# Performance work log

Measured on AMD Instinct MI355X. Metric: run time of the kernel, lower is better.

The kernel has to match this reference:

```python
import jax, jax.numpy as jnp
import numpy as np
from jax import lax
from jax.scipy.special import logsumexp

B, S, H, L = 64, 512, 1024, 9

def setup_inputs() -> dict:
    key = jax.random.key(0)
    ks = jax.random.split(key, 7)
    return {
        'sequence_output': jax.random.normal(ks[0], (B, S, H), dtype=jnp.float32),
        'tags': jax.random.randint(ks[1], (B, S), 0, L, dtype=jnp.int32),
        'mask': jnp.ones((B, S), dtype=bool),
        'W': jax.random.normal(ks[2], (L, H), dtype=jnp.float32) * 0.02,
        'b': jax.random.normal(ks[3], (L,), dtype=jnp.float32) * 0.02,
        'start_transitions': jax.random.normal(ks[4], (L,), dtype=jnp.float32) * 0.1,
        'end_transitions': jax.random.normal(ks[5], (L,), dtype=jnp.float32) * 0.1,
        'transitions': jax.random.normal(ks[6], (L,), dtype=jnp.float32).repeat(1) if False else jax.random.normal(ks[6], (L, L), dtype=jnp.float32) * 0.1,
    }

def _crf_nll(emissions, tags, mask, start_transitions, end_transitions, transitions):
    # emissions: [B,S,L], tags: [B,S] int, mask: [B,S] bool (mask[:,0] all True)
    Bn, Sn, Ln = emissions.shape
    maskf = mask.astype(emissions.dtype)
    bidx = jnp.arange(Bn)
    # ---- numerator: score of the gold tag sequence ----
    score = start_transitions[tags[:, 0]] + emissions[bidx, 0, tags[:, 0]]
    trans_sc = transitions[tags[:, :-1], tags[:, 1:]]                      # [B,S-1]
    emit_sc = jnp.take_along_axis(emissions, tags[..., None].astype(jnp.int32), axis=2)[..., 0]  # [B,S]
    score = score + jnp.sum((trans_sc + emit_sc[:, 1:]) * maskf[:, 1:], axis=1)
    seq_ends = jnp.sum(mask.astype(jnp.int32), axis=1) - 1                 # [B]
    last_tags = tags[bidx, seq_ends]
    score = score + end_transitions[last_tags]
    # ---- denominator: log partition via forward algorithm (scan over time) ----
    em_t = jnp.swapaxes(emissions, 0, 1)   # [S,B,L]
    mk_t = jnp.swapaxes(mask, 0, 1)        # [S,B]
    alpha0 = start_transitions + em_t[0]   # [B,L]
    def step(alpha, xs):
        em, m = xs
        nxt = logsumexp(alpha[:, :, None] + transitions[None] + em[:, None, :], axis=1)
        alpha = jnp.where(m[:, None], nxt, alpha)
        return alpha, None
    alpha, _ = lax.scan(step, alpha0, (em_t[1:], mk_t[1:]))
    logZ = logsumexp(alpha + end_transitions, axis=1)  # [B]
    llh = jnp.sum(score - logZ)  # reduction='sum'
    return -llh

def reference(sequence_output, tags, mask, W, b, start_transitions, end_transitions, transitions):
    # dropout is identity in eval/reference mode
    emissions = jnp.einsum('bsh,lh->bsl', sequence_output, W) + b
    return _crf_nll(emissions, tags, mask, start_transitions, end_transitions, transitions)
```

## Files before the change

kernel.cpp:

```cpp
#include <hip/hip_runtime.h>
#include <math.h>

#define Bn 64
#define Sn 512
#define Hn 1024
#define Ln 9
#define NC 32
#define KC 16

typedef __attribute__((ext_vector_type(8))) short bf16x8;
typedef __attribute__((ext_vector_type(4))) float f32x4;

__device__ __forceinline__ unsigned pack_bf16(float a, float b) {
  return (__float_as_uint(a) >> 16) | (__float_as_uint(b) & 0xFFFF0000u);
}

__global__ __launch_bounds__(256, 4) void crf_fused(
    const float* __restrict__ seq, const int* __restrict__ tags,
    const float* __restrict__ W, const float* __restrict__ bias,
    const float* __restrict__ startT, const float* __restrict__ endT,
    const float* __restrict__ trans, float* __restrict__ Mall,
    float* __restrict__ alphaBuf, float* __restrict__ out) {
  const int bc = blockIdx.x;
  const int b = bc >> 5, c = bc & (NC - 1);
  const int tid = threadIdx.x;
  const int lane = tid & 63;
  const int wv = tid >> 6;

  __shared__ float Clds[4][16][16];
  __shared__ float em_lds[KC][Ln];
  __shared__ float Mlds[2][Ln][12];

  const int t0 = c * KC;
  const int m = lane & 15;
  const int quad = lane >> 4;

  const float* arow = seq + ((size_t)b * Sn + t0 + m) * Hn;
  const bool bvalid = (m < Ln);
  const float* brow = W + (size_t)(bvalid ? m : 0) * Hn;

  f32x4 acc = {0.f, 0.f, 0.f, 0.f};
  const int ks = wv * 256;

#pragma unroll
  for (int it = 0; it < 8; ++it) {
    const int k0 = ks + it * 32 + quad * 8;
    float4 xa = *(const float4*)(arow + k0);
    float4 xb = *(const float4*)(arow + k0 + 4);
    float4 wa = *(const float4*)(brow + k0);
    float4 wb = *(const float4*)(brow + k0 + 4);

    union { bf16x8 v; unsigned u[4]; } af, bf;
    af.u[0] = pack_bf16(xa.x, xa.y);
    af.u[1] = pack_bf16(xa.z, xa.w);
    af.u[2] = pack_bf16(xb.x, xb.y);
    af.u[3] = pack_bf16(xb.z, xb.w);
    if (bvalid) {
      bf.u[0] = pack_bf16(wa.x, wa.y);
      bf.u[1] = pack_bf16(wa.z, wa.w);
      bf.u[2] = pack_bf16(wb.x, wb.y);
      bf.u[3] = pack_bf16(wb.z, wb.w);
    } else {
      bf.u[0] = bf.u[1] = bf.u[2] = bf.u[3] = 0u;
    }
    acc = __builtin_amdgcn_mfma_f32_16x16x32_bf16(af.v, bf.v, acc, 0, 0, 0);
  }

#pragma unroll
  for (int r = 0; r < 4; ++r) Clds[wv][quad * 4 + r][m] = acc[r];
  __syncthreads();

  if (tid < KC * Ln) {
    const int t = tid / Ln, l = tid - t * Ln;
    em_lds[t][l] = Clds[0][t][l] + Clds[1][t][l] + Clds[2][t][l] +
                   Clds[3][t][l] + bias[l];
  }
  __syncthreads();

  if (wv == 3) {
    float g = 0.f;
    if (lane < KC) {
      const int t = t0 + lane;
      const int cur = tags[b * Sn + t];
      const float e = em_lds[lane][cur];
      if (t == 0) {
        g = startT[cur] + e;
      } else {
        const int prev = tags[b * Sn + t - 1];
        g = trans[prev * Ln + cur] + e;
      }
      if (t == Sn - 1) g += endT[cur];
    }
#pragma unroll
    for (int off = 8; off > 0; off >>= 1) g += __shfl_xor(g, off);
    if (lane == 0) atomicAdd(out, -g);
  }

  if (c == 0) {
    if (wv == 0) {
      const int j = (lane < Ln) ? lane : 0;
      float Tcol[Ln];
#pragma unroll
      for (int i = 0; i < Ln; ++i) Tcol[i] = trans[i * Ln + j];
      float alpha[Ln];
#pragma unroll
      for (int i = 0; i < Ln; ++i) alpha[i] = startT[i] + em_lds[0][i];

      for (int t = 1; t < KC; ++t) {
        float mm = alpha[0];
#pragma unroll
        for (int i = 1; i < Ln; ++i) mm = fmaxf(mm, alpha[i]);
        float s = 0.f;
#pragma unroll
        for (int i = 0; i < Ln; ++i) s += __expf(alpha[i] - mm + Tcol[i]);
        float nxt = mm + __logf(s) + em_lds[t][j];
#pragma unroll
        for (int i = 0; i < Ln; ++i) alpha[i] = __shfl(nxt, i);
      }
      if (lane < Ln) alphaBuf[b * 16 + lane] = alpha[lane];
    }
  } else {
    const bool act = (tid < 81);
    const int i = tid / 9, j = tid - i * 9;
    float Treg[Ln];
    if (act) {
#pragma unroll
      for (int k = 0; k < Ln; ++k) Treg[k] = trans[k * Ln + j];
    }
    float val = 0.f;
    if (act) {
      val = trans[i * Ln + j] + em_lds[0][j];
      Mlds[0][i][j] = val;
    }
    __syncthreads();

    int cur = 0;
    for (int t = 1; t < KC; ++t) {
      if (act) {
        float Mr[Ln];
#pragma unroll
        for (int k = 0; k < Ln; ++k) Mr[k] = Mlds[cur][i][k];
        float e = em_lds[t][j];
        float mm = Mr[0];
#pragma unroll
        for (int k = 1; k < Ln; ++k) mm = fmaxf(mm, Mr[k]);
        float s = 0.f;
#pragma unroll
        for (int k = 0; k < Ln; ++k) s += __expf(Mr[k] - mm + Treg[k]);
        val = mm + __logf(s) + e;
        Mlds[cur ^ 1][i][j] = val;
      }
      __syncthreads();
      cur ^= 1;
    }
    if (act) Mall[(size_t)bc * 81 + tid] = val;
  }
}

__global__ __launch_bounds__(64) void crf_combine(
    const float* __restrict__ Mall, const float* __restrict__ alphaBuf,
    const float* __restrict__ endT, float* __restrict__ out) {
  const int b = blockIdx.x;
  const int lane = threadIdx.x;
  const int j = (lane < Ln) ? lane : 0;
  const float* Mb = Mall + (size_t)b * NC * 81;

  float alpha[Ln];
#pragma unroll
  for (int i = 0; i < Ln; ++i) alpha[i] = alphaBuf[b * 16 + i];

  float col[Ln];
#pragma unroll
  for (int i = 0; i < Ln; ++i) col[i] = Mb[81 + i * 9 + j];

  for (int cc = 1; cc < NC; ++cc) {
    float ncol[Ln];
    if (cc + 1 < NC) {
#pragma unroll
      for (int i = 0; i < Ln; ++i) ncol[i] = Mb[(cc + 1) * 81 + i * 9 + j];
    }
    float m = alpha[0];
#pragma unroll
    for (int i = 1; i < Ln; ++i) m = fmaxf(m, alpha[i]);
    float s = 0.f;
#pragma unroll
    for (int i = 0; i < Ln; ++i) s += __expf(alpha[i] - m + col[i]);
    float nxt = m + __logf(s);
#pragma unroll
    for (int i = 0; i < Ln; ++i) alpha[i] = __shfl(nxt, i);
#pragma unroll
    for (int i = 0; i < Ln; ++i) col[i] = ncol[i];
  }

  float mf = alpha[0] + endT[0];
#pragma unroll
  for (int i = 1; i < Ln; ++i) mf = fmaxf(mf, alpha[i] + endT[i]);
  float z = 0.f;
#pragma unroll
  for (int i = 0; i < Ln; ++i) z += __expf(alpha[i] + endT[i] - mf);
  float logZ = mf + __logf(z);

  if (lane == 0) atomicAdd(out, logZ);
}

extern "C" void kernel_launch(void* const* d_in, const int* in_sizes, int n_in,
                              void* d_out, int out_size, void* d_ws, size_t ws_size,
                              hipStream_t stream) {
  const float* seq    = (const float*)d_in[0];
  const int*   tags   = (const int*)d_in[1];
  const float* W      = (const float*)d_in[3];
  const float* bias   = (const float*)d_in[4];
  const float* startT = (const float*)d_in[5];
  const float* endT   = (const float*)d_in[6];
  const float* trans  = (const float*)d_in[7];

  float* Mall     = (float*)d_ws;
  float* alphaBuf = Mall + (size_t)Bn * NC * 81;

  crf_fused<<<Bn * NC, 256, 0, stream>>>(seq, tags, W, bias, startT, endT,
                                         trans, Mall, alphaBuf, (float*)d_out);
  crf_combine<<<Bn, 64, 0, stream>>>(Mall, alphaBuf, endT, (float*)d_out);
}
```

Measured before the change: 229.4 us.

## Stage sequence tile through LDS with coalesced row loads before MFMA

Activations were previously read straight from global memory: each lane fetched 32-byte pieces from 16 different rows. They are now loaded cooperatively in 256-column chunks with fully coalesced float4 reads into a padded shared-memory tile, and the MFMA operands are read from there. The goal is better DRAM coalescing on the bandwidth-bound read of sequence_output. In exchange it adds about 16KB of LDS, which may reduce occupancy, and two block barriers per chunk with no double buffering, so load latency is no longer hidden by unrolled independent loads.

```diff
diff --git a/kernel.cpp b/kernel.cpp
--- a/kernel.cpp
+++ b/kernel.cpp
@@ -7,6 +7,8 @@
 #define Ln 9
 #define NC 32
 #define KC 16
+#define KCH 256
+#define APAD 260
 
 typedef __attribute__((ext_vector_type(8))) short bf16x8;
 typedef __attribute__((ext_vector_type(4))) float f32x4;
@@ -27,6 +29,7 @@
   const int lane = tid & 63;
   const int wv = tid >> 6;
 
+  __shared__ float Axf[16][APAD];
   __shared__ float Clds[4][16][16];
   __shared__ float em_lds[KC][Ln];
   __shared__ float Mlds[2][Ln][12];
@@ -35,35 +38,52 @@
   const int m = lane & 15;
   const int quad = lane >> 4;
 
-  const float* arow = seq + ((size_t)b * Sn + t0 + m) * Hn;
   const bool bvalid = (m < Ln);
   const float* brow = W + (size_t)(bvalid ? m : 0) * Hn;
+  const float* xbase = seq + ((size_t)b * Sn + t0) * Hn;
 
   f32x4 acc = {0.f, 0.f, 0.f, 0.f};
-  const int ks = wv * 256;
-
-#pragma unroll
-  for (int it = 0; it < 8; ++it) {
-    const int k0 = ks + it * 32 + quad * 8;
-    float4 xa = *(const float4*)(arow + k0);
-    float4 xb = *(const float4*)(arow + k0 + 4);
-    float4 wa = *(const float4*)(brow + k0);
-    float4 wb = *(const float4*)(brow + k0 + 4);
-
-    union { bf16x8 v; unsigned u[4]; } af, bf;
-    af.u[0] = pack_bf16(xa.x, xa.y);
-    af.u[1] = pack_bf16(xa.z, xa.w);
-    af.u[2] = pack_bf16(xb.x, xb.y);
-    af.u[3] = pack_bf16(xb.z, xb.w);
-    if (bvalid) {
-      bf.u[0] = pack_bf16(wa.x, wa.y);
-      bf.u[1] = pack_bf16(wa.z, wa.w);
-      bf.u[2] = pack_bf16(wb.x, wb.y);
-      bf.u[3] = pack_bf16(wb.z, wb.w);
-    } else {
-      bf.u[0] = bf.u[1] = bf.u[2] = bf.u[3] = 0u;
-    }
-    acc = __builtin_amdgcn_mfma_f32_16x16x32_bf16(af.v, bf.v, acc, 0, 0, 0);
+
+#pragma unroll
+  for (int kc = 0; kc < Hn / KCH; ++kc) {
+#pragma unroll
+    for (int rep = 0; rep < 4; ++rep) {
+      const int fi = rep * 256 + tid;
+      const int row = fi >> 6;
+      const int c4 = fi & 63;
+      float4 v = *(const float4*)(xbase + (size_t)row * Hn + kc * KCH + c4 * 4);
+      *(float4*)&Axf[row][c4 * 4] = v;
+    }
+    __syncthreads();
+
+#pragma unroll
+    for (int h = 0; h < 2; ++h) {
+      const int kloc = wv * 64 + h * 32 + quad * 8;
+      const float* ap = &Axf[m][kloc];
+      float4 xa = *(const float4*)(ap);
+      float4 xb = *(const float4*)(ap + 4);
+      float4 wa, wb;
+      if (bvalid) {
+        wa = *(const float4*)(brow + kc * KCH + kloc);
+        wb = *(const float4*)(brow + kc * KCH + kloc + 4);
+      }
+
+      union { bf16x8 v; unsigned u[4]; } af, bf;
+      af.u[0] = pack_bf16(xa.x, xa.y);
+      af.u[1] = pack_bf16(xa.z, xa.w);
+      af.u[2] = pack_bf16(xb.x, xb.y);
+      af.u[3] = pack_bf16(xb.z, xb.w);
+      if (bvalid) {
+        bf.u[0] = pack_bf16(wa.x, wa.y);
+        bf.u[1] = pack_bf16(wa.z, wa.w);
+        bf.u[2] = pack_bf16(wb.x, wb.y);
+        bf.u[3] = pack_bf16(wb.z, wb.w);
+      } else {
+        bf.u[0] = bf.u[1] = bf.u[2] = bf.u[3] = 0u;
+      }
+      acc = __builtin_amdgcn_mfma_f32_16x16x32_bf16(af.v, bf.v, acc, 0, 0, 0);
+    }
+    __syncthreads();
   }
 
 #pragma unroll
```

Result: slower. 235.0 us (+2.5%).

## Split fused emission GEMM and CRF chunk scan into separate kernels

Applied to the files above, without the earlier changes.

Splits the fused kernel in two. The first kernel does only the bf16 MFMA emission projection and writes emissions to a global workspace. The second, a 128-thread kernel, reloads them to compute the gold-path score and the per-chunk transfer matrices. This keeps the serial 15-step chunk scan with its many barriers from holding GEMM blocks and their memory bandwidth. The cost is an extra kernel launch and a small global round trip for emissions.

```diff
diff --git a/kernel.cpp b/kernel.cpp
--- a/kernel.cpp
+++ b/kernel.cpp
@@ -15,12 +15,9 @@
   return (__float_as_uint(a) >> 16) | (__float_as_uint(b) & 0xFFFF0000u);
 }
 
-__global__ __launch_bounds__(256, 4) void crf_fused(
-    const float* __restrict__ seq, const int* __restrict__ tags,
-    const float* __restrict__ W, const float* __restrict__ bias,
-    const float* __restrict__ startT, const float* __restrict__ endT,
-    const float* __restrict__ trans, float* __restrict__ Mall,
-    float* __restrict__ alphaBuf, float* __restrict__ out) {
+__global__ __launch_bounds__(256) void emis_mfma(
+    const float* __restrict__ seq, const float* __restrict__ W,
+    const float* __restrict__ bias, float* __restrict__ em) {
   const int bc = blockIdx.x;
   const int b = bc >> 5, c = bc & (NC - 1);
   const int tid = threadIdx.x;
@@ -28,8 +25,6 @@
   const int wv = tid >> 6;
 
   __shared__ float Clds[4][16][16];
-  __shared__ float em_lds[KC][Ln];
-  __shared__ float Mlds[2][Ln][12];
 
   const int t0 = c * KC;
   const int m = lane & 15;
@@ -72,33 +67,49 @@
 
   if (tid < KC * Ln) {
     const int t = tid / Ln, l = tid - t * Ln;
-    em_lds[t][l] = Clds[0][t][l] + Clds[1][t][l] + Clds[2][t][l] +
-                   Clds[3][t][l] + bias[l];
-  }
+    em[((size_t)b * Sn + t0) * Ln + tid] =
+        Clds[0][t][l] + Clds[1][t][l] + Clds[2][t][l] + Clds[3][t][l] +
+        bias[l];
+  }
+}
+
+__global__ __launch_bounds__(128) void crf_chunk(
+    const float* __restrict__ em, const int* __restrict__ tags,
+    const float* __restrict__ trans, const float* __restrict__ startT,
+    const float* __restrict__ endT, float* __restrict__ Mall,
+    float* __restrict__ alphaBuf, float* __restrict__ out) {
+  const int bc = blockIdx.x;
+  const int b = bc >> 5, c = bc & (NC - 1);
+  const int tid = threadIdx.x;
+  const int t0 = c * KC;
+
+  __shared__ float em_lds[KC][Ln];
+  __shared__ float Mlds[2][Ln][12];
+
+  if (tid < KC * Ln)
+    ((float*)em_lds)[tid] = em[((size_t)b * Sn + t0) * Ln + tid];
   __syncthreads();
 
-  if (wv == 3) {
-    float g = 0.f;
-    if (lane < KC) {
-      const int t = t0 + lane;
-      const int cur = tags[b * Sn + t];
-      const float e = em_lds[lane][cur];
-      if (t == 0) {
-        g = startT[cur] + e;
-      } else {
-        const int prev = tags[b * Sn + t - 1];
-        g = trans[prev * Ln + cur] + e;
-      }
-      if (t == Sn - 1) g += endT[cur];
-    }
+  if (tid >= 96 && tid < 112) {
+    const int tt = tid - 96;
+    const int t = t0 + tt;
+    const int cur = tags[b * Sn + t];
+    float g = em_lds[tt][cur];
+    if (t == 0) {
+      g += startT[cur];
+    } else {
+      const int prev = tags[b * Sn + t - 1];
+      g += trans[prev * Ln + cur];
+    }
+    if (t == Sn - 1) g += endT[cur];
 #pragma unroll
     for (int off = 8; off > 0; off >>= 1) g += __shfl_xor(g, off);
-    if (lane == 0) atomicAdd(out, -g);
+    if (tt == 0) atomicAdd(out, -g);
   }
 
   if (c == 0) {
-    if (wv == 0) {
-      const int j = (lane < Ln) ? lane : 0;
+    if (tid < 64) {
+      const int j = (tid < Ln) ? tid : 0;
       float Tcol[Ln];
 #pragma unroll
       for (int i = 0; i < Ln; ++i) Tcol[i] = trans[i * Ln + j];
@@ -117,7 +128,7 @@
 #pragma unroll
         for (int i = 0; i < Ln; ++i) alpha[i] = __shfl(nxt, i);
       }
-      if (lane < Ln) alphaBuf[b * 16 + lane] = alpha[lane];
+      if (tid < Ln) alphaBuf[b * 16 + tid] = alpha[tid];
     }
   } else {
     const bool act = (tid < 81);
@@ -214,10 +225,12 @@
   const float* endT   = (const float*)d_in[6];
   const float* trans  = (const float*)d_in[7];
 
-  float* Mall     = (float*)d_ws;
+  float* em       = (float*)d_ws;
+  float* Mall     = em + (size_t)Bn * Sn * Ln;
   float* alphaBuf = Mall + (size_t)Bn * NC * 81;
 
-  crf_fused<<<Bn * NC, 256, 0, stream>>>(seq, tags, W, bias, startT, endT,
-                                         trans, Mall, alphaBuf, (float*)d_out);
+  emis_mfma<<<Bn * NC, 256, 0, stream>>>(seq, W, bias, em);
+  crf_chunk<<<Bn * NC, 128, 0, stream>>>(em, tags, trans, startT, endT,
+                                         Mall, alphaBuf, (float*)d_out);
   crf_combine<<<Bn, 64, 0, stream>>>(Mall, alphaBuf, endT, (float*)d_out);
 }
```

Result: slower. 253.4 us (+10.5%).
